# Kernel tuning notes

Measured on AMD Instinct MI355X. Metric: run time of the kernel, lower is better.

Reference implementation:

```python
import jax, jax.numpy as jnp
import numpy as np


def _conv1x1(x, W, b):
    # x: [B,C,H,W] (NCHW), W: [out,in] (1x1 conv kernel), b: [out]
    return jnp.einsum('bchw,oc->bohw', x, W) + b[None, :, None, None]


def setup_inputs() -> dict:
    key = jax.random.key(0)
    ks = jax.random.split(key, 12)
    B, C, H, W = 8, 256, 64, 64
    s = 1.0 / np.sqrt(C)
    x = jax.random.normal(ks[0], (B, C, H, W), dtype=jnp.float32)
    mask = jnp.round(jax.random.uniform(ks[1], (B, 1, H, W), dtype=jnp.float32))
    Wq = jax.random.normal(ks[2], (C, C), dtype=jnp.float32) * s
    bq = jax.random.normal(ks[3], (C,), dtype=jnp.float32) * 0.01
    Wk = jax.random.normal(ks[4], (C, C), dtype=jnp.float32) * s
    bk = jax.random.normal(ks[5], (C,), dtype=jnp.float32) * 0.01
    Wv = jax.random.normal(ks[6], (C, C), dtype=jnp.float32) * s
    bv = jax.random.normal(ks[7], (C,), dtype=jnp.float32) * 0.01
    Wo = jax.random.normal(ks[8], (C, C), dtype=jnp.float32) * s
    bo = jax.random.normal(ks[9], (C,), dtype=jnp.float32) * 0.01
    gamma = jnp.zeros((1,), dtype=jnp.float32)
    return {"input": x, "mask": mask, "Wq": Wq, "bq": bq, "Wk": Wk, "bk": bk,
            "Wv": Wv, "bv": bv, "Wo": Wo, "bo": bo, "gamma": gamma}


def reference(input, mask, Wq, bq, Wk, bk, Wv, bv, Wo, bo, gamma):
    B, C, H, W = input.shape
    # mask spatial size matches input -> no avg_pool branch (pre_feat is None)
    feat_f = input * mask            # foreground features -> queries
    feat_b = input * (1.0 - mask)    # background features -> keys/values
    q = _conv1x1(feat_f, Wq, bq).reshape(B, C, -1)   # [B,C,N]
    k = _conv1x1(feat_b, Wk, bk).reshape(B, C, -1)   # [B,C,N]
    v = _conv1x1(feat_b, Wv, bv).reshape(B, C, -1)   # [B,C,N]
    # scores[b,n,m] = q[:,n]^T k[:,m]  (no scaling, matching the torch code)
    scores = jnp.einsum('bcn,bcm->bnm', q, k)        # [B,N,N]
    attn = jax.nn.softmax(scores, axis=-1)
    out = jnp.einsum('bnm,bcm->bcn', attn, v).reshape(B, C, H, W)
    out = _conv1x1(out, Wo, bo)
    return out + gamma * input
```

## Files before the change

kernel.cpp:

```cpp
#include <hip/hip_runtime.h>

#define CC 256
#define NN 4096
#define NB 8
#define NM ((size_t)CC * NN)

#define OFF_OVF   589824
#define OFF_LM    720896
#define OFF_POSM  739328
#define OFF_POSF  747520
#define OFF_CNT   755712
#define OFF_W16   755776
#define PMAIN     524288
#define QCAP      2304

typedef _Float16 f16;
typedef f16 f16x4 __attribute__((ext_vector_type(4)));
typedef f16 f16x8 __attribute__((ext_vector_type(8)));
typedef float f32x4 __attribute__((ext_vector_type(4)));
typedef unsigned int u32;

__global__ __launch_bounds__(256) void prep_kernel(
    const float* __restrict__ Wq, const float* __restrict__ Wk,
    const float* __restrict__ Wv, const float* __restrict__ Wo,
    const float* __restrict__ mask, f16* __restrict__ wsh, int b0)
{
    const int blk = blockIdx.x;
    const int t = threadIdx.x;
    if (blk < 64) {
        f16* w16 = wsh + OFF_W16;
        int i = (blk * 256 + t) * 4;
        float4 a = *(const float4*)(Wq + i);
        float4 b = *(const float4*)(Wk + i);
        float4 c = *(const float4*)(Wv + i);
        float4 d = *(const float4*)(Wo + i);
        f16x4 ha, hb, hc, hd;
        ha[0]=(f16)a.x; ha[1]=(f16)a.y; ha[2]=(f16)a.z; ha[3]=(f16)a.w;
        hb[0]=(f16)b.x; hb[1]=(f16)b.y; hb[2]=(f16)b.z; hb[3]=(f16)b.w;
        hc[0]=(f16)c.x; hc[1]=(f16)c.y; hc[2]=(f16)c.z; hc[3]=(f16)c.w;
        hd[0]=(f16)d.x; hd[1]=(f16)d.y; hd[2]=(f16)d.z; hd[3]=(f16)d.w;
        *(f16x4*)(w16 + i)            = ha;
        *(f16x4*)(w16 + 65536 + i)    = hb;
        *(f16x4*)(w16 + 131072 + i)   = hc;
        *(f16x4*)(w16 + 196608 + i)   = hd;
        return;
    }
    const int slot = blk - 64;
    const int b = b0 + slot;
    const int lane = t & 63, w = t >> 6;
    __shared__ int wsum0[4], wsum1[4];
    const float* mp = mask + (size_t)b * NN;
    f16* base = wsh + (size_t)slot * 4 * NM;
    int* pm = (int*)(base + OFF_POSM);
    int* pf = (int*)(base + OFF_POSF);
    int* cn = (int*)(base + OFF_CNT);

    int loc0[16], loc1[16], c0 = 0, c1 = 0;
    float mv[16];
#pragma unroll
    for (int i = 0; i < 16; ++i) {
        mv[i] = mp[t * 16 + i];
        loc0[i] = c0; loc1[i] = c1;
        if (mv[i] == 0.0f) ++c0; else ++c1;
    }
    int i0 = c0, i1 = c1;
#pragma unroll
    for (int d = 1; d < 64; d <<= 1) {
        int v0 = __shfl_up(i0, d, 64);
        int v1 = __shfl_up(i1, d, 64);
        if (lane >= d) { i0 += v0; i1 += v1; }
    }
    if (lane == 63) { wsum0[w] = i0; wsum1[w] = i1; }
    int e0 = i0 - c0, e1 = i1 - c1;
    __syncthreads();
    int s0 = e0, s1 = e1;
    for (int i = 0; i < w; ++i) { s0 += wsum0[i]; s1 += wsum1[i]; }
#pragma unroll
    for (int i = 0; i < 16; ++i) {
        pm[t * 16 + i] = (mv[i] == 0.0f) ? (s0 + loc0[i]) : -1;
        pf[t * 16 + i] = (mv[i] != 0.0f) ? (s1 + loc1[i]) : -1;
    }
    if (t == 0) {
        cn[0] = wsum0[0] + wsum0[1] + wsum0[2] + wsum0[3];
        cn[1] = wsum1[0] + wsum1[1] + wsum1[2] + wsum1[3];
    }
}

__global__ __launch_bounds__(512, 4) void proj_fused_kernel(
    const float* __restrict__ x, const float* __restrict__ mask,
    const f16* __restrict__ w16, const float* __restrict__ bq,
    const float* __restrict__ bk, const float* __restrict__ bv,
    f16* __restrict__ wsh, int b0)
{
    __shared__ f16x8 xf[2048];
    __shared__ f16x8 xb[2048];

    const int t = threadIdx.x;
    const int lane = t & 63, w = t >> 6;
    const int l16 = lane & 15, quad = lane >> 4;
    const int slot = blockIdx.x;
    const int b = b0 + slot;
    const int n0 = blockIdx.y * 64;
    const float* xp = x + (size_t)b * NM;
    f16* base = wsh + (size_t)slot * 4 * NM;
    const int* pom = (const int*)(base + OFF_POSM);
    const int* pof = (const int*)(base + OFF_POSF);
    const int* cn  = (const int*)(base + OFF_CNT);

    float mf  = mask[(size_t)b * NN + n0 + lane];
    float mbk = 1.0f - mf;
#pragma unroll
    for (int i = 0; i < 4; ++i) {
        int cb = w * 4 + i;
        const float* col = xp + (size_t)cb * 8 * NN + n0 + lane;
        f16x8 vf, vb;
#pragma unroll
        for (int u = 0; u < 8; ++u) {
            float xv = col[(size_t)u * NN];
            vf[u] = (f16)(xv * mf);
            vb[u] = (f16)(xv * mbk);
        }
        int unit = ((cb >> 2) * 4 + (lane >> 4)) * 64 + (cb & 3) * 16 + (lane & 15);
        xf[unit] = vf;
        xb[unit] = vb;
    }
    __syncthreads();

#pragma unroll
    for (int pr = 0; pr < 3; ++pr) {
        int j0  = w * 6 + pr * 2;
        int p   = j0 >> 4;
        int oc0 = j0 & 15;
        const f16* Wp     = w16 + (size_t)p * 65536;
        const float* bias = (p == 0) ? bq : (p == 1) ? bk : bv;
        const f16x8* bt   = (p == 0) ? xf : xb;

        f16x8 wf[2][8];
#pragma unroll
        for (int h = 0; h < 2; ++h) {
            const f16* wrow = Wp + (size_t)((oc0 + h) * 16 + l16) * CC + quad * 8;
#pragma unroll
            for (int kc = 0; kc < 8; ++kc)
                wf[h][kc] = *(const f16x8*)(wrow + kc * 32);
        }
        f32x4 acc[2][4];
#pragma unroll
        for (int h = 0; h < 2; ++h)
#pragma unroll
            for (int nc = 0; nc < 4; ++nc) acc[h][nc] = (f32x4){0.f, 0.f, 0.f, 0.f};
#pragma unroll
        for (int nc = 0; nc < 4; ++nc)
#pragma unroll
            for (int kc = 0; kc < 8; ++kc) {
                f16x8 bf = bt[(kc * 4 + nc) * 64 + lane];
                acc[0][nc] = __builtin_amdgcn_mfma_f32_16x16x32_f16(wf[0][kc], bf, acc[0][nc], 0, 0, 0);
                acc[1][nc] = __builtin_amdgcn_mfma_f32_16x16x32_f16(wf[1][kc], bf, acc[1][nc], 0, 0, 0);
            }
#pragma unroll
        for (int h = 0; h < 2; ++h) {
            int oc = oc0 + h;
            float bvv[4];
#pragma unroll
            for (int r = 0; r < 4; ++r) bvv[r] = bias[oc * 16 + quad * 4 + r];
            if (p == 2) {
                f16* vpl = base + 2 * NM;
#pragma unroll
                for (int nc = 0; nc < 4; ++nc) {
                    int cp = pom[n0 + nc * 16 + l16];
                    if (cp >= 0) {
#pragma unroll
                        for (int r = 0; r < 4; ++r)
                            vpl[(size_t)(oc * 16 + quad * 4 + r) * NN + cp] =
                                (f16)(acc[h][nc][r] + bvv[r]);
                    }
                }
            } else if (p == 1) {
                f16* kpl = base + NM;
#pragma unroll
                for (int nc = 0; nc < 4; ++nc) {
                    int cp = pom[n0 + nc * 16 + l16];
                    if (cp >= 0) {
                        f16x4 pk;
#pragma unroll
                        for (int r = 0; r < 4; ++r) pk[r] = (f16)(acc[h][nc][r] + bvv[r]);
                        *(f16x4*)(kpl + (size_t)cp * CC + oc * 16 + quad * 4) = pk;
                    }
                }
            } else {
#pragma unroll
                for (int nc = 0; nc < 4; ++nc) {
                    int cp = pof[n0 + nc * 16 + l16];
                    if (cp >= 0) {
                        f16x4 pk;
#pragma unroll
                        for (int r = 0; r < 4; ++r) pk[r] = (f16)(acc[h][nc][r] + bvv[r]);
                        *(f16x4*)(base + (size_t)cp * CC + oc * 16 + quad * 4) = pk;
                    }
                }
            }
        }
    }

    if (blockIdx.y == 0) {
        int Fb = cn[0], Ff = cn[1];
        f16x8 z8;
#pragma unroll
        for (int i = 0; i < 8; ++i) z8[i] = (f16)0.0f;
        {
            int Mp = (Fb + 31) & ~31;
            int pad = Mp - Fb;
            if (pad > 0) {
                f16* kpl = base + NM;
                f16* vpl = base + 2 * NM;
                for (int idx = t; idx < pad * 32; idx += 512)
                    *(f16x8*)(kpl + (size_t)(Fb + idx / 32) * CC + (idx & 31) * 8) = z8;
                for (int idx = t; idx < pad * CC; idx += 512)
                    vpl[(size_t)(idx / pad) * NN + Fb + (idx % pad)] = (f16)0.0f;
            }
        }
        for (int c = t; c < CC; c += 512)
            base[(size_t)Ff * CC + c] = (f16)bq[c];
        {
            int qe = (Ff + 64) & ~63;
            int nz = qe - (Ff + 1);
            for (int idx = t; idx < nz * 32; idx += 512)
                *(f16x8*)(base + (size_t)(Ff + 1 + idx / 32) * CC + (idx & 31) * 8) = z8;
        }
    }
}

__global__ __launch_bounds__(256, 2) void flash_kernel(
    f16* __restrict__ wsh, const float* __restrict__ bk,
    const float* __restrict__ bv, int b0)
{
    __shared__ f16x8 klds[1024];
    __shared__ f16x8 vlds[1024];
    __shared__ f16 pbuf[4][16 * 40];

    const int t    = threadIdx.x;
    const int w    = t >> 6;
    const int lane = t & 63;
    const int l16  = lane & 15;
    const int quad = lane >> 4;
    const int slot = blockIdx.x;
    const int n0   = (blockIdx.y >> 1) * 64;
    const int z    = blockIdx.y & 1;

    f16* base = wsh + (size_t)slot * 4 * NM;
    const int* cn = (const int*)(base + OFF_CNT);
    const int Fb = cn[0], Ff = cn[1];
    if (n0 > Ff) return;

    const f16* qt = base;
    const f16* kt = base + NM;
    const f16* vp = base + 2 * NM;

    const int nt  = (Fb + 31) >> 5;
    const int h   = (nt + 1) >> 1;
    const int mt0 = z ? h : 0;
    const int mt1 = z ? nt : h;

    int koff[4], voff[4];
#pragma unroll
    for (int i = 0; i < 4; ++i) {
        int u = i * 256 + t;
        koff[i] = (((u >> 9) & 1) * 16 + (u & 15)) * CC
                + ((u >> 6) & 7) * 32 + ((u >> 4) & 3) * 8;
        voff[i] = ((u >> 6) * 16 + (u & 15)) * NN + ((u >> 4) & 3) * 8;
    }

    const int nrow = n0 + w * 16 + l16;
    f16x8 qf[8];
#pragma unroll
    for (int kc = 0; kc < 8; ++kc)
        qf[kc] = *(const f16x8*)(qt + (size_t)nrow * CC + kc * 32 + quad * 8);

    f32x4 oacc[17];
#pragma unroll
    for (int i = 0; i < 17; ++i) oacc[i] = (f32x4){0.f, 0.f, 0.f, 0.f};
    float M[4] = {-3.0e38f, -3.0e38f, -3.0e38f, -3.0e38f};

    f16* pw = &pbuf[w][0];
    f16x8 ones;
#pragma unroll
    for (int i = 0; i < 8; ++i) ones[i] = (f16)1.0f;

    f16x8 kreg[4], vreg[4];
    if (mt1 > mt0) {
#pragma unroll
        for (int i = 0; i < 4; ++i) {
            kreg[i] = *(const f16x8*)(kt + (size_t)(mt0 * 32) * CC + koff[i]);
            vreg[i] = *(const f16x8*)(vp + (size_t)(mt0 * 32) + voff[i]);
        }
    }

    for (int it = mt0; it < mt1; ++it) {
#pragma unroll
        for (int i = 0; i < 4; ++i) {
            klds[i * 256 + t] = kreg[i];
            vlds[i * 256 + t] = vreg[i];
        }
        __syncthreads();
        if (it + 1 < mt1) {
#pragma unroll
            for (int i = 0; i < 4; ++i) {
                kreg[i] = *(const f16x8*)(kt + (size_t)((it + 1) * 32) * CC + koff[i]);
                vreg[i] = *(const f16x8*)(vp + (size_t)((it + 1) * 32) + voff[i]);
            }
        }

        f32x4 s[2];
        s[0] = (f32x4){0.f, 0.f, 0.f, 0.f};
        s[1] = (f32x4){0.f, 0.f, 0.f, 0.f};
        __builtin_amdgcn_s_setprio(1);
#pragma unroll
        for (int kc = 0; kc < 8; ++kc) {
            f16x8 k0 = klds[kc * 64 + lane];
            f16x8 k1 = klds[(8 + kc) * 64 + lane];
            s[0] = __builtin_amdgcn_mfma_f32_16x16x32_f16(qf[kc], k0, s[0], 0, 0, 0);
            s[1] = __builtin_amdgcn_mfma_f32_16x16x32_f16(qf[kc], k1, s[1], 0, 0, 0);
        }
        __builtin_amdgcn_s_setprio(0);

        if (((it + 1) << 5) > Fb) {
#pragma unroll
            for (int ms = 0; ms < 2; ++ms)
                if (it * 32 + ms * 16 + l16 >= Fb) {
#pragma unroll
                    for (int r = 0; r < 4; ++r) s[ms][r] = -3.0e38f;
                }
        }

        bool up = false;
#pragma unroll
        for (int ms = 0; ms < 2; ++ms)
#pragma unroll
            for (int r = 0; r < 4; ++r) up |= (s[ms][r] > M[r] + 8.0f);
        if (__any(up)) {
            float alpha[4];
#pragma unroll
            for (int r = 0; r < 4; ++r) {
                float tm = fmaxf(s[0][r], s[1][r]);
                tm = fmaxf(tm, __shfl_xor(tm, 1, 64));
                tm = fmaxf(tm, __shfl_xor(tm, 2, 64));
                tm = fmaxf(tm, __shfl_xor(tm, 4, 64));
                tm = fmaxf(tm, __shfl_xor(tm, 8, 64));
                float Mn = fmaxf(M[r], tm);
                alpha[r] = __expf(M[r] - Mn);
                M[r] = Mn;
            }
#pragma unroll
            for (int cs = 0; cs < 17; ++cs)
#pragma unroll
                for (int r = 0; r < 4; ++r) oacc[cs][r] *= alpha[r];
        }
#pragma unroll
        for (int ms = 0; ms < 2; ++ms)
#pragma unroll
            for (int r = 0; r < 4; ++r)
                pw[(quad * 4 + r) * 40 + ms * 16 + l16] = (f16)__expf(s[ms][r] - M[r]);
        asm volatile("s_waitcnt lgkmcnt(0)" ::: "memory");
        f16x8 pf = *(const f16x8*)(pw + l16 * 40 + quad * 8);

        __builtin_amdgcn_s_setprio(1);
#pragma unroll
        for (int cs = 0; cs < 16; ++cs) {
            f16x8 vf = vlds[cs * 64 + lane];
            oacc[cs] = __builtin_amdgcn_mfma_f32_16x16x32_f16(pf, vf, oacc[cs], 0, 0, 0);
        }
        oacc[16] = __builtin_amdgcn_mfma_f32_16x16x32_f16(pf, ones, oacc[16], 0, 0, 0);
        __builtin_amdgcn_s_setprio(0);

        __syncthreads();
    }

    if (z == 0) {
        float cnn = 0.f;
#pragma unroll
        for (int kc = 0; kc < 8; ++kc) {
            const float* bkp = bk + kc * 32 + quad * 8;
#pragma unroll
            for (int j = 0; j < 8; ++j)
                cnn += (float)qf[kc][j] * bkp[j];
        }
        cnn += __shfl_xor(cnn, 16, 64);
        cnn += __shfl_xor(cnn, 32, 64);
        const float Ffw = (float)Ff;
        float aw[4], wv[4];
#pragma unroll
        for (int r = 0; r < 4; ++r) {
            float cr = __shfl(cnn, quad * 4 + r, 64);
            float Mn = fmaxf(M[r], cr);
            aw[r] = __expf(M[r] - Mn);
            wv[r] = Ffw * __expf(cr - Mn);
            M[r] = Mn;
        }
#pragma unroll
        for (int cs = 0; cs < 16; ++cs) {
            float bvc = bv[cs * 16 + l16];
#pragma unroll
            for (int r = 0; r < 4; ++r)
                oacc[cs][r] = oacc[cs][r] * aw[r] + wv[r] * bvc;
        }
#pragma unroll
        for (int r = 0; r < 4; ++r)
            oacc[16][r] = oacc[16][r] * aw[r] + wv[r];
    }

    float inv[4];
#pragma unroll
    for (int r = 0; r < 4; ++r) {
        float Lr = oacc[16][r];
        inv[r] = (Lr > 0.f) ? 1.0f / Lr : 0.f;
    }
#pragma unroll
    for (int r = 0; r < 4; ++r) {
        int row = n0 + w * 16 + quad * 4 + r;
        f16* pp = (row < 2048)
                ? base + 3 * NM + (size_t)z * PMAIN + (size_t)row * 256
                : base + OFF_OVF + (size_t)z * 65536 + (size_t)(row - 2048) * 256;
#pragma unroll
        for (int cs = 0; cs < 16; ++cs)
            pp[cs * 16 + l16] = (f16)(oacc[cs][r] * inv[r]);
    }
    if (l16 == 0) {
        float* LMw = (float*)(base + OFF_LM);
#pragma unroll
        for (int r = 0; r < 4; ++r) {
            int row = n0 + w * 16 + quad * 4 + r;
            LMw[((size_t)z * QCAP + row) * 2 + 0] = oacc[16][r];
            LMw[((size_t)z * QCAP + row) * 2 + 1] = M[r];
        }
    }
}

__global__ __launch_bounds__(512, 4) void combine_kernel(
    const f16* __restrict__ wsh, const float* __restrict__ bo,
    const float* __restrict__ x, const float* __restrict__ gamma,
    float* __restrict__ outall, int b0)
{
    __shared__ f16x8 ot[2048];

    const int t = threadIdx.x;
    const int lane = t & 63, w = t >> 6;
    const int l16 = lane & 15, quad = lane >> 4;
    const int slot = blockIdx.x;
    const int b = b0 + slot;
    const int n0 = blockIdx.y * 64;

    const f16* base = wsh + (size_t)slot * 4 * NM;
    const int* pof = (const int*)(base + OFF_POSF);
    const int* cn  = (const int*)(base + OFF_CNT);
    const int Ff = cn[1];
    const float* LMp = (const float*)(base + OFF_LM);
    const f16* wo16 = wsh + OFF_W16 + (size_t)3 * 65536;

#pragma unroll
    for (int i = 0; i < 4; ++i) {
        int u = i * 512 + t;
        int ul16 = u & 15, uq = (u >> 4) & 3, unc = (u >> 6) & 3, ukc = u >> 8;
        int orign = n0 + unc * 16 + ul16;
        int pfv = pof[orign];
        int crow = (pfv >= 0) ? pfv : Ff;
        int c0 = ukc * 32 + uq * 8;
        const f16* p0 = (crow < 2048)
                      ? base + 3 * NM + (size_t)crow * 256
                      : base + OFF_OVF + (size_t)(crow - 2048) * 256;
        const f16* p1 = (crow < 2048)
                      ? base + 3 * NM + PMAIN + (size_t)crow * 256
                      : base + OFF_OVF + 65536 + (size_t)(crow - 2048) * 256;
        f16x8 o0 = *(const f16x8*)(p0 + c0);
        f16x8 o1 = *(const f16x8*)(p1 + c0);
        float L0 = LMp[(size_t)crow * 2], M0 = LMp[(size_t)crow * 2 + 1];
        float L1 = LMp[((size_t)QCAP + crow) * 2], M1 = LMp[((size_t)QCAP + crow) * 2 + 1];
        float Mx = fmaxf(M0, M1);
        float w0 = L0 * __expf(M0 - Mx);
        float w1 = L1 * __expf(M1 - Mx);
        float inv = 1.0f / (w0 + w1);
        f16x8 om;
#pragma unroll
        for (int j = 0; j < 8; ++j)
            om[j] = (f16)((w0 * (float)o0[j] + w1 * (float)o1[j]) * inv);
        ot[u] = om;
    }
    __syncthreads();

    const float* xp = x + (size_t)b * NM;
    float* outp = outall + (size_t)b * NM;
    float g = gamma[0];
    {
        int oc0 = w * 2;
        f16x8 wf[2][8];
#pragma unroll
        for (int h = 0; h < 2; ++h) {
            const f16* wrow = wo16 + (size_t)((oc0 + h) * 16 + l16) * CC + quad * 8;
#pragma unroll
            for (int kc = 0; kc < 8; ++kc)
                wf[h][kc] = *(const f16x8*)(wrow + kc * 32);
        }
        f32x4 acc[2][4];
#pragma unroll
        for (int h = 0; h < 2; ++h)
#pragma unroll
            for (int nc = 0; nc < 4; ++nc) acc[h][nc] = (f32x4){0.f, 0.f, 0.f, 0.f};
#pragma unroll
        for (int nc = 0; nc < 4; ++nc)
#pragma unroll
            for (int kc = 0; kc < 8; ++kc) {
                f16x8 bf = ot[(kc * 4 + nc) * 64 + lane];
                acc[0][nc] = __builtin_amdgcn_mfma_f32_16x16x32_f16(wf[0][kc], bf, acc[0][nc], 0, 0, 0);
                acc[1][nc] = __builtin_amdgcn_mfma_f32_16x16x32_f16(wf[1][kc], bf, acc[1][nc], 0, 0, 0);
            }
#pragma unroll
        for (int h = 0; h < 2; ++h) {
            int oc = oc0 + h;
            float bvv[4];
#pragma unroll
            for (int r = 0; r < 4; ++r) bvv[r] = bo[oc * 16 + quad * 4 + r];
#pragma unroll
            for (int nc = 0; nc < 4; ++nc)
#pragma unroll
                for (int r = 0; r < 4; ++r) {
                    size_t o = oc * 16 + quad * 4 + r;
                    size_t n = n0 + nc * 16 + l16;
                    outp[o * NN + n] = acc[h][nc][r] + bvv[r] + g * xp[o * NN + n];
                }
        }
    }
}

__global__ __launch_bounds__(256) void ones_kernel(float* __restrict__ out, int total)
{
    for (int i = blockIdx.x * 256 + threadIdx.x; i < total; i += gridDim.x * 256)
        out[i] = 1.0f;
}

extern "C" void kernel_launch(void* const* d_in, const int* in_sizes, int n_in,
                              void* d_out, int out_size, void* d_ws, size_t ws_size,
                              hipStream_t stream)
{
    const float* x     = (const float*)d_in[0];
    const float* mask  = (const float*)d_in[1];
    const float* Wq    = (const float*)d_in[2];
    const float* bq    = (const float*)d_in[3];
    const float* Wk    = (const float*)d_in[4];
    const float* bk    = (const float*)d_in[5];
    const float* Wv    = (const float*)d_in[6];
    const float* bv    = (const float*)d_in[7];
    const float* Wo    = (const float*)d_in[8];
    const float* bo    = (const float*)d_in[9];
    const float* gamma = (const float*)d_in[10];
    float* out = (float*)d_out;

    const size_t slot_bytes = 4 * NM * sizeof(f16);
    f16* wsh = (f16*)d_ws;
    int nb = (int)(ws_size / slot_bytes);
    if (nb < 1) {
        ones_kernel<<<2048, 256, 0, stream>>>(out, out_size);
        return;
    }
    if (nb > NB) nb = NB;

    f16* w16 = wsh + OFF_W16;

    for (int b0 = 0; b0 < NB; b0 += nb) {
        int nbc = NB - b0; if (nbc > nb) nbc = nb;
        prep_kernel<<<64 + nbc, 256, 0, stream>>>(Wq, Wk, Wv, Wo, mask, wsh, b0);
        dim3 gP(nbc, NN / 64);
        dim3 gF(nbc, (QCAP / 64) * 2);
        dim3 gC(nbc, NN / 64);
        proj_fused_kernel<<<gP, 512, 0, stream>>>(x, mask, w16, bq, bk, bv, wsh, b0);
        flash_kernel<<<gF, 256, 0, stream>>>(wsh, bk, bv, b0);
        combine_kernel<<<gC, 512, 0, stream>>>(wsh, bo, x, gamma, out, b0);
    }
}
```

Measured before the change: 273.8 us.

## Stage V projection tile in LDS and write compacted background columns coalesced

```diff
diff --git a/kernel.cpp b/kernel.cpp
--- a/kernel.cpp
+++ b/kernel.cpp
@@ -94,6 +94,8 @@
 {
     __shared__ f16x8 xf[2048];
     __shared__ f16x8 xb[2048];
+    __shared__ int bgl[64];
+    __shared__ int vmeta[2];
 
     const int t = threadIdx.x;
     const int lane = t & 63, w = t >> 6;
@@ -106,6 +108,7 @@
     const int* pom = (const int*)(base + OFF_POSM);
     const int* pof = (const int*)(base + OFF_POSF);
     const int* cn  = (const int*)(base + OFF_CNT);
+    f16* vtile = (f16*)xf;
 
     float mf  = mask[(size_t)b * NN + n0 + lane];
     float mbk = 1.0f - mf;
@@ -124,12 +127,23 @@
         xf[unit] = vf;
         xb[unit] = vb;
     }
+    if (w == 0) {
+        int p = pom[n0 + lane];
+        unsigned long long bal = __ballot(p >= 0);
+        int nbg = __popcll(bal);
+        int pmn = (p >= 0) ? p : 0x7fffffff;
+#pragma unroll
+        for (int d = 32; d > 0; d >>= 1) pmn = min(pmn, __shfl_xor(pmn, d, 64));
+        if (p >= 0) bgl[p - pmn] = lane;
+        if (lane == 0) { vmeta[0] = pmn; vmeta[1] = nbg; }
+    }
     __syncthreads();
 
 #pragma unroll
     for (int pr = 0; pr < 3; ++pr) {
-        int j0  = w * 6 + pr * 2;
-        int p   = j0 >> 4;
+        if (pr == 1) __syncthreads();
+        int j0  = pr * 16 + w * 2;
+        int p   = pr;
         int oc0 = j0 & 15;
         const f16* Wp     = w16 + (size_t)p * 65536;
         const float* bias = (p == 0) ? bq : (p == 1) ? bk : bv;
@@ -163,17 +177,12 @@
 #pragma unroll
             for (int r = 0; r < 4; ++r) bvv[r] = bias[oc * 16 + quad * 4 + r];
             if (p == 2) {
-                f16* vpl = base + 2 * NM;
-#pragma unroll
-                for (int nc = 0; nc < 4; ++nc) {
-                    int cp = pom[n0 + nc * 16 + l16];
-                    if (cp >= 0) {
-#pragma unroll
-                        for (int r = 0; r < 4; ++r)
-                            vpl[(size_t)(oc * 16 + quad * 4 + r) * NN + cp] =
-                                (f16)(acc[h][nc][r] + bvv[r]);
-                    }
-                }
+#pragma unroll
+                for (int nc = 0; nc < 4; ++nc)
+#pragma unroll
+                    for (int r = 0; r < 4; ++r)
+                        vtile[(oc * 16 + quad * 4 + r) * 64 + nc * 16 + l16] =
+                            (f16)(acc[h][nc][r] + bvv[r]);
             } else if (p == 1) {
                 f16* kpl = base + NM;
 #pragma unroll
@@ -197,6 +206,21 @@
                         *(f16x4*)(base + (size_t)cp * CC + oc * 16 + quad * 4) = pk;
                     }
                 }
+            }
+        }
+    }
+    __syncthreads();
+
+    {
+        int cp0 = vmeta[0], nbg = vmeta[1];
+        f16* vpl = base + 2 * NM;
+        int i = t & 63;
+        if (i < nbg) {
+            int ln = bgl[i];
+#pragma unroll
+            for (int pass = 0; pass < 32; ++pass) {
+                int c = pass * 8 + (t >> 6);
+                vpl[(size_t)c * NN + cp0 + i] = vtile[c * 64 + ln];
             }
         }
     }
```

Result: slower. 282.9 us (+3.3%).
